# Kernel tuning notes

Hardware: AMD Instinct MI355X
Metric: run time of the kernel (lower is better)

The kernel has to match this reference:

```python
import jax, jax.numpy as jnp
import numpy as np
from jax import lax

B, CIN, IMG = 32, 3, 128   # batch, image channels, image size
D, K = 256, 512            # codebook dim, codebook size


def _conv(x, w, stride, pad):
    # PyTorch Conv2d (bias=False), NCHW / OIHW
    return lax.conv_general_dilated(x, w, (stride, stride), ((pad, pad), (pad, pad)),
                                    dimension_numbers=('NCHW', 'OIHW', 'NCHW'))


def _deconv(x, w, b):
    # PyTorch ConvTranspose2d(k=4, s=2, p=1): lhs_dilation=2, pad=k-1-p=2, flipped kernel,
    # weight layout (in, out, kh, kw) -> 'IOHW'
    y = lax.conv_general_dilated(x, jnp.flip(w, (2, 3)), (1, 1), ((2, 2), (2, 2)),
                                 lhs_dilation=(2, 2),
                                 dimension_numbers=('NCHW', 'IOHW', 'NCHW'))
    return y + b[None, :, None, None]


def _res(x, w1, w2):
    # Faithful to the source ResidualBlock: relu1 output is DISCARDED (conv1 applied to x)
    out = _conv(x, w1, 1, 1)      # 3x3, pad 1
    out = jax.nn.relu(out)
    out = _conv(out, w2, 1, 0)    # 1x1, pad 0
    return out + x


def setup_inputs() -> dict:
    key = jax.random.key(0)
    ks = jax.random.split(key, 20)
    s = 0.05
    inp = {
        'x': jax.random.uniform(ks[0], (B, CIN, IMG, IMG), jnp.float32),
        # codebook, init uniform(-1/K, 1/K) as in init_weights
        'embed_w': jax.random.uniform(ks[1], (K, D), jnp.float32, -1.0 / K, 1.0 / K),
        # encoder
        'e_w1': jax.random.normal(ks[2], (D, CIN, 4, 4), jnp.float32) * s,
        'e_w2': jax.random.normal(ks[3], (D, D, 4, 4), jnp.float32) * s,
        'e_r1a': jax.random.normal(ks[4], (D, D, 3, 3), jnp.float32) * s,
        'e_r1b': jax.random.normal(ks[5], (D, D, 1, 1), jnp.float32) * s,
        'e_r2a': jax.random.normal(ks[6], (D, D, 3, 3), jnp.float32) * s,
        'e_r2b': jax.random.normal(ks[7], (D, D, 1, 1), jnp.float32) * s,
        # decoder
        'd_r1a': jax.random.normal(ks[8], (D, D, 3, 3), jnp.float32) * s,
        'd_r1b': jax.random.normal(ks[9], (D, D, 1, 1), jnp.float32) * s,
        'd_r2a': jax.random.normal(ks[10], (D, D, 3, 3), jnp.float32) * s,
        'd_r2b': jax.random.normal(ks[11], (D, D, 1, 1), jnp.float32) * s,
        'dt1_w': jax.random.normal(ks[12], (D, D, 4, 4), jnp.float32) * s,  # (in,out,kh,kw)
        'dt1_b': jnp.zeros((D,), jnp.float32),
        'dt2_w': jax.random.normal(ks[13], (D, CIN, 4, 4), jnp.float32) * s,
        'dt2_b': jnp.zeros((CIN,), jnp.float32),
    }
    return inp


def reference(x, embed_w, e_w1, e_w2, e_r1a, e_r1b, e_r2a, e_r2b,
              d_r1a, d_r1b, d_r2a, d_r2b, dt1_w, dt1_b, dt2_w, dt2_b):
    # ---- encoder (BN layers exist but are never called in the source forward) ----
    h = jax.nn.relu(_conv(x, e_w1, 2, 1))          # (B,D,64,64)
    h = jax.nn.relu(_conv(h, e_w2, 2, 1))          # (B,D,32,32)
    h = _res(h, e_r1a, e_r1b)
    z_e = _res(h, e_r2a, e_r2b)                    # (B,D,H,W)

    # ---- vector quantisation ----
    ze = jnp.transpose(z_e, (0, 2, 3, 1))          # (B,H,W,D)
    # squared L2 distances via expansion (same argmin/values as the broadcast diff tensor)
    d2 = (jnp.sum(ze * ze, -1, keepdims=True)      # (B,H,W,1)
          - 2.0 * jnp.einsum('bhwd,kd->bhwk', ze, embed_w)
          + jnp.sum(embed_w * embed_w, -1))        # (B,H,W,K)
    dist = jnp.sqrt(jnp.maximum(d2, 0.0))          # torch.norm(p=2) before min
    idx = jnp.argmin(dist, axis=-1)                # (B,H,W)
    z_q = embed_w[idx]                             # (B,H,W,D) gather

    # losses: source averages over an extra duplicated K axis, identical to mean over B,H,W
    sg = lax.stop_gradient
    loss1 = jnp.mean(jnp.sum((ze - sg(z_q)) ** 2, -1))   # grads -> encoder
    loss2 = jnp.mean(jnp.sum((sg(ze) - z_q) ** 2, -1))   # grads -> codebook

    # ---- decoder (takes z_q; BN layers never called; relu after deconv1 only) ----
    dq = jnp.transpose(z_q, (0, 3, 1, 2))          # (B,D,H,W)
    dq = _res(dq, d_r1a, d_r1b)
    dq = _res(dq, d_r2a, d_r2b)
    dq = jax.nn.relu(_deconv(dq, dt1_w, dt1_b))    # (B,D,64,64)
    recon = jax.nn.sigmoid(_deconv(dq, dt2_w, dt2_b))  # (B,3,128,128)
    return recon, loss1, loss2
```

## Files before the change

kernel.cpp:

```cpp
#include <hip/hip_runtime.h>


typedef __attribute__((ext_vector_type(8))) short bf16x8;
typedef __attribute__((ext_vector_type(4))) float f32x4;
#define MFMA_B16(a, b, c) __builtin_amdgcn_mfma_f32_16x16x32_bf16(a, b, c, 0, 0, 0)

__device__ inline unsigned short f2b(float f) {
    unsigned int u = __float_as_uint(f);
    unsigned int r = u + 0x7fffu + ((u >> 16) & 1u);
    return (unsigned short)(r >> 16);
}
__device__ inline float b2f(unsigned short u) {
    return __uint_as_float(((unsigned int)u) << 16);
}

struct PermfArgs {
    const float* src[10];
    int kw[10];
    int so[10], si[10], sh[10], sw[10];
    int cum[11];
};

__global__ void permf_all_k(PermfArgs a, unsigned short* __restrict__ dst)
{
    int gid = blockIdx.x * 256 + threadIdx.x;
    if (gid >= a.cum[10]) return;
    int seg = 0;
    while (seg < 9 && gid >= a.cum[seg + 1]) ++seg;
    int l = gid - a.cum[seg];
    int q = l & 31;
    int n = (l >> 5) & 255;
    int rest = l >> 13;
    int cch = rest & 7;
    int khkw = rest >> 3;
    int kh = khkw / a.kw[seg], kw = khkw % a.kw[seg];
    int ci = cch * 32 + q;
    dst[gid] = f2b(a.src[seg][n * a.so[seg] + ci * a.si[seg] + kh * a.sh[seg] + kw * a.sw[seg]]);
}

__global__ void misc_prep_k(const float* __restrict__ dt2_w, unsigned short* __restrict__ wg,
                            const float* __restrict__ embed, unsigned short* __restrict__ embF,
                            const float* __restrict__ e_w1, unsigned short* __restrict__ wgc,
                            float* __restrict__ nrm, float* __restrict__ lacc)
{
    int blk = blockIdx.x, tid = threadIdx.x;
    if (blk < 48) {
        int idx = blk * 256 + tid;
        int q = idx & 31;
        int n = (idx >> 5) % 48;
        int cch = idx / (48 * 32);
        int ci = cch * 32 + q;
        int oc = n % 3, khkw = n / 3;
        int kh = khkw >> 2, kw = khkw & 3;
        wg[idx] = f2b(dt2_w[ci * 48 + oc * 16 + kh * 4 + kw]);
    } else if (blk < 560) {
        int idx = (blk - 48) * 256 + tid;
        int q = idx & 31;
        int n = (idx >> 5) & 511;
        int cch = idx >> 14;
        embF[idx] = f2b(embed[n * 256 + cch * 32 + q]);
    } else if (blk < 624) {
        int idx = (blk - 560) * 256 + tid;
        int q = idx & 31;
        int n = (idx >> 5) & 255;
        int kt = idx >> 13;
        int k = kt * 32 + q;
        float v = 0.f;
        if (k < 48) {
            int ci = k >> 4, kh = (k >> 2) & 3, kwv = k & 3;
            v = e_w1[n * 48 + ci * 16 + kh * 4 + kwv];
        }
        wgc[idx] = f2b(v);
    } else if (blk < 752) {
        int row = (blk - 624) * 4 + (tid >> 6);
        int lane = tid & 63;
        float s = 0.f;
        #pragma unroll
        for (int c = 0; c < 256; c += 64) {
            float v = embed[row * 256 + c + lane];
            s += v * v;
        }
        #pragma unroll
        for (int off = 1; off < 64; off <<= 1) s += __shfl_xor(s, off);
        if (lane == 0) nrm[row] = s;
    } else {
        if (tid == 0) lacc[0] = 0.f;
    }
}

__global__ void lossfin_k(const float* __restrict__ lacc, float* __restrict__ out)
{
    if (threadIdx.x == 0) {
        float m = lacc[0] * (1.0f / 32768.0f);
        out[1572864] = m;
        out[1572865] = m;
    }
}

__global__ void __launch_bounds__(256, 4)
conv1m_k(const float* __restrict__ x, const unsigned short* __restrict__ wgc,
         unsigned short* __restrict__ out)
{
    int bh = blockIdx.x;
    int b = bh >> 6, oh = bh & 63;
    int tid = threadIdx.x;
    int lane = tid & 63, wv = tid >> 6;
    int m = lane & 15, quad = lane >> 4;
    __shared__ float xrow[3][4][130];
    __shared__ __align__(16) unsigned short imc[64 * 72];
    for (int s = tid; s < 1560; s += 256) {
        int col = s % 130;
        int t = s / 130;
        int r = t & 3;
        int c = t >> 2;
        int ih = 2 * oh - 1 + r, iw = col - 1;
        float v = 0.f;
        if ((unsigned)ih < 128u && (unsigned)iw < 128u)
            v = x[(((b * 3 + c) << 7) + ih) * 128 + iw];
        xrow[c][r][col] = v;
    }
    __syncthreads();
    for (int s = tid; s < 4096; s += 256) {
        int px = s >> 6, k = s & 63;
        float v = 0.f;
        if (k < 48) {
            int ci = k >> 4, kh = (k >> 2) & 3, kw = k & 3;
            v = xrow[ci][kh][2 * px + kw];
        }
        imc[px * 72 + k] = f2b(v);
    }
    __syncthreads();
    f32x4 acc[16];
    f32x4 z = {0.f, 0.f, 0.f, 0.f};
    #pragma unroll
    for (int i = 0; i < 16; ++i) acc[i] = z;
    bf16x8 a0 = *(const bf16x8*)&imc[((wv << 4) + m) * 72 + (quad << 3)];
    bf16x8 a1 = *(const bf16x8*)&imc[((wv << 4) + m) * 72 + 32 + (quad << 3)];
    #pragma unroll
    for (int nt = 0; nt < 16; ++nt) {
        bf16x8 b0 = *(const bf16x8*)&wgc[(nt * 16 + m) * 32 + (quad << 3)];
        bf16x8 b1 = *(const bf16x8*)&wgc[(256 + nt * 16 + m) * 32 + (quad << 3)];
        acc[nt] = MFMA_B16(a0, b0, acc[nt]);
        acc[nt] = MFMA_B16(a1, b1, acc[nt]);
    }
    #pragma unroll
    for (int nt = 0; nt < 16; ++nt)
        #pragma unroll
        for (int r = 0; r < 4; ++r) {
            int px = (wv << 4) + quad * 4 + r;
            out[(((bh << 6) + px) << 8) + nt * 16 + (lane & 15)] = f2b(fmaxf(acc[nt][r], 0.f));
        }
}

__global__ void __launch_bounds__(256, 3)
mconv2_k(const unsigned short* __restrict__ in, const unsigned short* __restrict__ wf,
         unsigned short* __restrict__ out)
{
    int blk = blockIdx.x;
    int bb = blk >> 4, j = blk & 15;
    int lane = threadIdx.x & 63;
    int n0 = (threadIdx.x >> 6) << 6;
    int m = lane & 15, quad = lane >> 4;
    __shared__ __align__(16) unsigned short win[2 * 66 * 132];
    f32x4 acc[2][2][4];
    f32x4 z = {0.f, 0.f, 0.f, 0.f};
    #pragma unroll
    for (int a = 0; a < 2; ++a)
        #pragma unroll
        for (int i = 0; i < 2; ++i)
            #pragma unroll
            for (int t = 0; t < 4; ++t) acc[a][i][t] = z;

    for (int c0 = 0; c0 < 256; c0 += 128) {
        for (int kh = 0; kh < 4; ++kh) {
            __syncthreads();
            for (int s = threadIdx.x; s < 2 * 66 * 16; s += 256) {
                int c16 = s & 15;
                int t2 = s >> 4;
                int col = t2 % 66;
                int rr = t2 / 66;
                int ih = 4 * j - 1 + kh + 2 * rr, iw = col - 1;
                int4 v = make_int4(0, 0, 0, 0);
                if ((unsigned)ih < 64u && (unsigned)iw < 64u)
                    v = *(const int4*)&in[((((bb << 6) + ih) << 6) + iw) * 256 + c0 + (c16 << 3)];
                int cs = (col >> 1) + (col & 1) * 33;
                *(int4*)&win[(rr * 66 + cs) * 132 + (c16 << 3)] = v;
            }
            __syncthreads();
            #pragma unroll
            for (int kw = 0; kw < 4; ++kw) {
                int csoff = (kw >> 1) + (kw & 1) * 33;
                #pragma unroll
                for (int cch = 0; cch < 4; ++cch) {
                    bf16x8 a00 = *(const bf16x8*)&win[(m + csoff) * 132 + (cch << 5) + (quad << 3)];
                    bf16x8 a01 = *(const bf16x8*)&win[(m + 16 + csoff) * 132 + (cch << 5) + (quad << 3)];
                    bf16x8 a10 = *(const bf16x8*)&win[(66 + m + csoff) * 132 + (cch << 5) + (quad << 3)];
                    bf16x8 a11 = *(const bf16x8*)&win[(66 + m + 16 + csoff) * 132 + (cch << 5) + (quad << 3)];
                    int cg = (c0 >> 5) + cch;
                    int wbase = ((((kh << 2) + kw) * 8 + cg) * 256 + n0 + m) * 32 + (quad << 3);
                    bf16x8 b0 = *(const bf16x8*)&wf[wbase];
                    bf16x8 b1 = *(const bf16x8*)&wf[wbase + 16 * 32];
                    bf16x8 b2 = *(const bf16x8*)&wf[wbase + 32 * 32];
                    bf16x8 b3 = *(const bf16x8*)&wf[wbase + 48 * 32];
                    acc[0][0][0] = MFMA_B16(a00, b0, acc[0][0][0]);
                    acc[0][0][1] = MFMA_B16(a00, b1, acc[0][0][1]);
                    acc[0][0][2] = MFMA_B16(a00, b2, acc[0][0][2]);
                    acc[0][0][3] = MFMA_B16(a00, b3, acc[0][0][3]);
                    acc[0][1][0] = MFMA_B16(a01, b0, acc[0][1][0]);
                    acc[0][1][1] = MFMA_B16(a01, b1, acc[0][1][1]);
                    acc[0][1][2] = MFMA_B16(a01, b2, acc[0][1][2]);
                    acc[0][1][3] = MFMA_B16(a01, b3, acc[0][1][3]);
                    acc[1][0][0] = MFMA_B16(a10, b0, acc[1][0][0]);
                    acc[1][0][1] = MFMA_B16(a10, b1, acc[1][0][1]);
                    acc[1][0][2] = MFMA_B16(a10, b2, acc[1][0][2]);
                    acc[1][0][3] = MFMA_B16(a10, b3, acc[1][0][3]);
                    acc[1][1][0] = MFMA_B16(a11, b0, acc[1][1][0]);
                    acc[1][1][1] = MFMA_B16(a11, b1, acc[1][1][1]);
                    acc[1][1][2] = MFMA_B16(a11, b2, acc[1][1][2]);
                    acc[1][1][3] = MFMA_B16(a11, b3, acc[1][1][3]);
                }
            }
        }
    }
    #pragma unroll
    for (int row = 0; row < 2; ++row) {
        int oh = 2 * j + row;
        #pragma unroll
        for (int mt = 0; mt < 2; ++mt)
            #pragma unroll
            for (int nt = 0; nt < 4; ++nt)
                #pragma unroll
                for (int r = 0; r < 4; ++r) {
                    int px = mt * 16 + quad * 4 + r;
                    int col = n0 + nt * 16 + m;
                    out[((((bb << 5) + oh) << 5) + px) * 256 + col] = f2b(fmaxf(acc[row][mt][nt][r], 0.f));
                }
    }
}

__global__ void __launch_bounds__(256, 3)
mconv3_k(const unsigned short* __restrict__ in, const unsigned short* __restrict__ wf,
         unsigned short* __restrict__ out)
{
    int blk = blockIdx.x;
    int bb = blk >> 4, j = blk & 15;
    int lane = threadIdx.x & 63;
    int n0 = (threadIdx.x >> 6) << 6;
    int m = lane & 15, quad = lane >> 4;
    __shared__ __align__(16) unsigned short win[4 * 34 * 132];
    f32x4 acc[2][2][4];
    f32x4 z = {0.f, 0.f, 0.f, 0.f};
    #pragma unroll
    for (int a = 0; a < 2; ++a)
        #pragma unroll
        for (int i = 0; i < 2; ++i)
            #pragma unroll
            for (int t = 0; t < 4; ++t) acc[a][i][t] = z;

    for (int c0 = 0; c0 < 256; c0 += 128) {
        __syncthreads();
        for (int s = threadIdx.x; s < 4 * 34 * 16; s += 256) {
            int c16 = s & 15;
            int t2 = s >> 4;
            int col = t2 % 34;
            int rr = t2 / 34;
            int ih = 2 * j - 1 + rr, iw = col - 1;
            int4 v = make_int4(0, 0, 0, 0);
            if ((unsigned)ih < 32u && (unsigned)iw < 32u)
                v = *(const int4*)&in[((((bb << 5) + ih) << 5) + iw) * 256 + c0 + (c16 << 3)];
            *(int4*)&win[(rr * 34 + col) * 132 + (c16 << 3)] = v;
        }
        __syncthreads();
        for (int kh = 0; kh < 3; ++kh) {
            #pragma unroll
            for (int kw = 0; kw < 3; ++kw) {
                #pragma unroll
                for (int cch = 0; cch < 4; ++cch) {
                    const unsigned short* ba = &win[(kh * 34 + m + kw) * 132 + (cch << 5) + (quad << 3)];
                    bf16x8 a00 = *(const bf16x8*)ba;
                    bf16x8 a01 = *(const bf16x8*)(ba + 16 * 132);
                    bf16x8 a10 = *(const bf16x8*)(ba + 34 * 132);
                    bf16x8 a11 = *(const bf16x8*)(ba + 50 * 132);
                    int cg = (c0 >> 5) + cch;
                    int wbase = (((kh * 3 + kw) * 8 + cg) * 256 + n0 + m) * 32 + (quad << 3);
                    bf16x8 b0 = *(const bf16x8*)&wf[wbase];
                    bf16x8 b1 = *(const bf16x8*)&wf[wbase + 16 * 32];
                    bf16x8 b2 = *(const bf16x8*)&wf[wbase + 32 * 32];
                    bf16x8 b3 = *(const bf16x8*)&wf[wbase + 48 * 32];
                    acc[0][0][0] = MFMA_B16(a00, b0, acc[0][0][0]);
                    acc[0][0][1] = MFMA_B16(a00, b1, acc[0][0][1]);
                    acc[0][0][2] = MFMA_B16(a00, b2, acc[0][0][2]);
                    acc[0][0][3] = MFMA_B16(a00, b3, acc[0][0][3]);
                    acc[0][1][0] = MFMA_B16(a01, b0, acc[0][1][0]);
                    acc[0][1][1] = MFMA_B16(a01, b1, acc[0][1][1]);
                    acc[0][1][2] = MFMA_B16(a01, b2, acc[0][1][2]);
                    acc[0][1][3] = MFMA_B16(a01, b3, acc[0][1][3]);
                    acc[1][0][0] = MFMA_B16(a10, b0, acc[1][0][0]);
                    acc[1][0][1] = MFMA_B16(a10, b1, acc[1][0][1]);
                    acc[1][0][2] = MFMA_B16(a10, b2, acc[1][0][2]);
                    acc[1][0][3] = MFMA_B16(a10, b3, acc[1][0][3]);
                    acc[1][1][0] = MFMA_B16(a11, b0, acc[1][1][0]);
                    acc[1][1][1] = MFMA_B16(a11, b1, acc[1][1][1]);
                    acc[1][1][2] = MFMA_B16(a11, b2, acc[1][1][2]);
                    acc[1][1][3] = MFMA_B16(a11, b3, acc[1][1][3]);
                }
            }
        }
    }
    #pragma unroll
    for (int row = 0; row < 2; ++row) {
        int oh = 2 * j + row;
        #pragma unroll
        for (int mt = 0; mt < 2; ++mt)
            #pragma unroll
            for (int nt = 0; nt < 4; ++nt)
                #pragma unroll
                for (int r = 0; r < 4; ++r) {
                    int px = mt * 16 + quad * 4 + r;
                    int col = n0 + nt * 16 + m;
                    out[((((bb << 5) + oh) << 5) + px) * 256 + col] = f2b(fmaxf(acc[row][mt][nt][r], 0.f));
                }
    }
}

__global__ void __launch_bounds__(256, 3)
m1x1_k(const unsigned short* __restrict__ in, const unsigned short* __restrict__ wf,
       const unsigned short* __restrict__ res, unsigned short* __restrict__ outb,
       float* __restrict__ outf, int f32out)
{
    int blk = blockIdx.x;
    int lane = threadIdx.x & 63;
    int n0 = (threadIdx.x >> 6) << 6;
    int m = lane & 15, quad = lane >> 4;
    __shared__ __align__(16) unsigned short win[64 * 264];
    f32x4 acc[4][4];
    f32x4 z = {0.f, 0.f, 0.f, 0.f};
    #pragma unroll
    for (int i = 0; i < 4; ++i)
        #pragma unroll
        for (int t = 0; t < 4; ++t) acc[i][t] = z;

    int rowbase = blk << 14;
    for (int s = threadIdx.x; s < 64 * 32; s += 256) {
        int c8 = s & 31, col = s >> 5;
        *(int4*)&win[col * 264 + (c8 << 3)] = *(const int4*)&in[rowbase + (col << 8) + (c8 << 3)];
    }
    __syncthreads();
    #pragma unroll
    for (int cch = 0; cch < 8; ++cch) {
        bf16x8 a0 = *(const bf16x8*)&win[m * 264 + (cch << 5) + (quad << 3)];
        bf16x8 a1 = *(const bf16x8*)&win[(m + 16) * 264 + (cch << 5) + (quad << 3)];
        bf16x8 a2 = *(const bf16x8*)&win[(m + 32) * 264 + (cch << 5) + (quad << 3)];
        bf16x8 a3 = *(const bf16x8*)&win[(m + 48) * 264 + (cch << 5) + (quad << 3)];
        int wbase = (cch * 256 + n0 + m) * 32 + (quad << 3);
        bf16x8 b0 = *(const bf16x8*)&wf[wbase];
        bf16x8 b1 = *(const bf16x8*)&wf[wbase + 16 * 32];
        bf16x8 b2 = *(const bf16x8*)&wf[wbase + 32 * 32];
        bf16x8 b3 = *(const bf16x8*)&wf[wbase + 48 * 32];
        acc[0][0] = MFMA_B16(a0, b0, acc[0][0]);
        acc[0][1] = MFMA_B16(a0, b1, acc[0][1]);
        acc[0][2] = MFMA_B16(a0, b2, acc[0][2]);
        acc[0][3] = MFMA_B16(a0, b3, acc[0][3]);
        acc[1][0] = MFMA_B16(a1, b0, acc[1][0]);
        acc[1][1] = MFMA_B16(a1, b1, acc[1][1]);
        acc[1][2] = MFMA_B16(a1, b2, acc[1][2]);
        acc[1][3] = MFMA_B16(a1, b3, acc[1][3]);
        acc[2][0] = MFMA_B16(a2, b0, acc[2][0]);
        acc[2][1] = MFMA_B16(a2, b1, acc[2][1]);
        acc[2][2] = MFMA_B16(a2, b2, acc[2][2]);
        acc[2][3] = MFMA_B16(a2, b3, acc[2][3]);
        acc[3][0] = MFMA_B16(a3, b0, acc[3][0]);
        acc[3][1] = MFMA_B16(a3, b1, acc[3][1]);
        acc[3][2] = MFMA_B16(a3, b2, acc[3][2]);
        acc[3][3] = MFMA_B16(a3, b3, acc[3][3]);
    }
    #pragma unroll
    for (int mt = 0; mt < 4; ++mt)
        #pragma unroll
        for (int nt = 0; nt < 4; ++nt)
            #pragma unroll
            for (int r = 0; r < 4; ++r) {
                int px = mt * 16 + quad * 4 + r;
                int col = n0 + nt * 16 + m;
                int idx = rowbase + (px << 8) + col;
                float v = acc[mt][nt][r] + b2f(res[idx]);
                outb[idx] = f2b(v);
                if (f32out) outf[idx] = v;
            }
}

__global__ void __launch_bounds__(256, 3)
mdeconv1_k(const unsigned short* __restrict__ in, const unsigned short* __restrict__ wf,
           const float* __restrict__ bias, unsigned short* __restrict__ out)
{
    int blk = blockIdx.x;
    int bb = blk >> 5;
    int rem = blk & 31;
    int pp = rem >> 4;
    int i = rem & 15;
    int oy_a = pp + 4 * i;
    int p = (oy_a + 1) & 1;
    int r0a = (oy_a + 1 - p) >> 1;
    int rbase = r0a - 1;
    int lane = threadIdx.x & 63;
    int n0 = (threadIdx.x >> 6) << 6;
    int m = lane & 15, quad = lane >> 4;
    __shared__ __align__(16) unsigned short win[3 * 34 * 264];

    for (int s = threadIdx.x; s < 3 * 34 * 32; s += 256) {
        int c8 = s & 31;
        int t2 = s >> 5;
        int col = t2 % 34;
        int rr = t2 / 34;
        int ih = rbase + rr, iw = col - 1;
        int4 v = make_int4(0, 0, 0, 0);
        if ((unsigned)ih < 32u && (unsigned)iw < 32u)
            v = *(const int4*)&in[((((bb << 5) + ih) << 5) + iw) * 256 + (c8 << 3)];
        *(int4*)&win[(rr * 34 + col) * 264 + (c8 << 3)] = v;
    }
    __syncthreads();

    for (int par = 0; par < 2; ++par) {
        f32x4 acc[2][2][4];
        f32x4 z = {0.f, 0.f, 0.f, 0.f};
        #pragma unroll
        for (int a = 0; a < 2; ++a)
            #pragma unroll
            for (int i2 = 0; i2 < 2; ++i2)
                #pragma unroll
                for (int t = 0; t < 4; ++t) acc[a][i2][t] = z;

        #pragma unroll
        for (int t = 0; t < 2; ++t) {
            int kh = p + 2 * t;
            #pragma unroll
            for (int u = 0; u < 2; ++u) {
                int kw = (1 - par) + 2 * u;
                int ixoff = par - u + 1;
                #pragma unroll
                for (int cch = 0; cch < 8; ++cch) {
                    const unsigned short* baA = &win[((1 - t) * 34 + m + ixoff) * 264 + (cch << 5) + (quad << 3)];
                    const unsigned short* baB = baA + 34 * 264;
                    bf16x8 a00 = *(const bf16x8*)baA;
                    bf16x8 a01 = *(const bf16x8*)(baA + 16 * 264);
                    bf16x8 a10 = *(const bf16x8*)baB;
                    bf16x8 a11 = *(const bf16x8*)(baB + 16 * 264);
                    int wbase = ((((kh << 2) + kw) * 8 + cch) * 256 + n0 + m) * 32 + (quad << 3);
                    bf16x8 b0 = *(const bf16x8*)&wf[wbase];
                    bf16x8 b1 = *(const bf16x8*)&wf[wbase + 16 * 32];
                    bf16x8 b2 = *(const bf16x8*)&wf[wbase + 32 * 32];
                    bf16x8 b3 = *(const bf16x8*)&wf[wbase + 48 * 32];
                    acc[0][0][0] = MFMA_B16(a00, b0, acc[0][0][0]);
                    acc[0][0][1] = MFMA_B16(a00, b1, acc[0][0][1]);
                    acc[0][0][2] = MFMA_B16(a00, b2, acc[0][0][2]);
                    acc[0][0][3] = MFMA_B16(a00, b3, acc[0][0][3]);
                    acc[0][1][0] = MFMA_B16(a01, b0, acc[0][1][0]);
                    acc[0][1][1] = MFMA_B16(a01, b1, acc[0][1][1]);
                    acc[0][1][2] = MFMA_B16(a01, b2, acc[0][1][2]);
                    acc[0][1][3] = MFMA_B16(a01, b3, acc[0][1][3]);
                    acc[1][0][0] = MFMA_B16(a10, b0, acc[1][0][0]);
                    acc[1][0][1] = MFMA_B16(a10, b1, acc[1][0][1]);
                    acc[1][0][2] = MFMA_B16(a10, b2, acc[1][0][2]);
                    acc[1][0][3] = MFMA_B16(a10, b3, acc[1][0][3]);
                    acc[1][1][0] = MFMA_B16(a11, b0, acc[1][1][0]);
                    acc[1][1][1] = MFMA_B16(a11, b1, acc[1][1][1]);
                    acc[1][1][2] = MFMA_B16(a11, b2, acc[1][1][2]);
                    acc[1][1][3] = MFMA_B16(a11, b3, acc[1][1][3]);
                }
            }
        }
        #pragma unroll
        for (int row = 0; row < 2; ++row) {
            int oy = oy_a + 2 * row;
            #pragma unroll
            for (int mt = 0; mt < 2; ++mt)
                #pragma unroll
                for (int nt = 0; nt < 4; ++nt) {
                    int col = n0 + nt * 16 + m;
                    float bs = bias[col];
                    #pragma unroll
                    for (int r = 0; r < 4; ++r) {
                        int ox = 2 * (mt * 16 + quad * 4 + r) + par;
                        float v = fmaxf(acc[row][mt][nt][r] + bs, 0.f);
                        out[((((bb << 6) + oy) << 6) + ox) * 256 + col] = f2b(v);
                    }
                }
        }
    }
}

__global__ void __launch_bounds__(256, 2)
vqm_k(const unsigned short* __restrict__ zeb, const float* __restrict__ zef,
      const unsigned short* __restrict__ embF, const float* __restrict__ embed,
      const float* __restrict__ nrm, unsigned short* __restrict__ zq,
      float* __restrict__ lacc)
{
    int bh = blockIdx.x;
    int tid = threadIdx.x;
    int lane = tid & 63;
    int wv = tid >> 6;
    int m = lane & 15, quad = lane >> 4;
    __shared__ __align__(16) unsigned short win[32 * 264];
    __shared__ float bvv[4][32];
    __shared__ int   bii[4][32];
    __shared__ int   bidx[32];
    int rowbase = bh << 13;
    for (int s = tid; s < 32 * 32; s += 256) {
        int c8 = s & 31, px = s >> 5;
        *(int4*)&win[px * 264 + (c8 << 3)] = *(const int4*)&zeb[rowbase + (px << 8) + (c8 << 3)];
    }
    __syncthreads();

    f32x4 acc[2][8];
    f32x4 z = {0.f, 0.f, 0.f, 0.f};
    #pragma unroll
    for (int i = 0; i < 2; ++i)
        #pragma unroll
        for (int j = 0; j < 8; ++j) acc[i][j] = z;

    #pragma unroll
    for (int cch = 0; cch < 8; ++cch) {
        bf16x8 a0 = *(const bf16x8*)&win[m * 264 + (cch << 5) + (quad << 3)];
        bf16x8 a1 = *(const bf16x8*)&win[(m + 16) * 264 + (cch << 5) + (quad << 3)];
        #pragma unroll
        for (int nt = 0; nt < 8; ++nt) {
            bf16x8 b = *(const bf16x8*)&embF[((cch << 9) + (wv << 7) + (nt << 4) + m) * 32 + (quad << 3)];
            acc[0][nt] = MFMA_B16(a0, b, acc[0][nt]);
            acc[1][nt] = MFMA_B16(a1, b, acc[1][nt]);
        }
    }

    float nv[8];
    #pragma unroll
    for (int nt = 0; nt < 8; ++nt) nv[nt] = nrm[(wv << 7) + (nt << 4) + m];

    #pragma unroll
    for (int mt = 0; mt < 2; ++mt)
        #pragma unroll
        for (int r = 0; r < 4; ++r) {
            float bv = 1e30f;
            int bi = 0x7fffffff;
            #pragma unroll
            for (int nt = 0; nt < 8; ++nt) {
                float d = nv[nt] - 2.f * acc[mt][nt][r];
                int n = (wv << 7) + (nt << 4) + m;
                if (d < bv || (d == bv && n < bi)) { bv = d; bi = n; }
            }
            #pragma unroll
            for (int off = 1; off < 16; off <<= 1) {
                float ov = __shfl_xor(bv, off);
                int oi = __shfl_xor(bi, off);
                if (ov < bv || (ov == bv && oi < bi)) { bv = ov; bi = oi; }
            }
            if (m == 0) {
                int px = mt * 16 + quad * 4 + r;
                bvv[wv][px] = bv;
                bii[wv][px] = bi;
            }
        }
    __syncthreads();
    if (tid < 32) {
        float bv = bvv[0][tid];
        int bi = bii[0][tid];
        #pragma unroll
        for (int w2 = 1; w2 < 4; ++w2) {
            float ov = bvv[w2][tid];
            int oi = bii[w2][tid];
            if (ov < bv || (ov == bv && oi < bi)) { bv = ov; bi = oi; }
        }
        bidx[tid] = bi;
    }
    __syncthreads();

    float lsum = 0.f;
    #pragma unroll
    for (int j = 0; j < 8; ++j) {
        int px = (wv << 3) + j;
        int bi = bidx[px];
        int pix = (bh << 5) + px;
        const float4 e = *(const float4*)&embed[bi * 256 + (lane << 2)];
        const float4 zv = *(const float4*)&zef[(pix << 8) + (lane << 2)];
        ushort4 eq;
        eq.x = f2b(e.x); eq.y = f2b(e.y); eq.z = f2b(e.z); eq.w = f2b(e.w);
        *(ushort4*)&zq[(pix << 8) + (lane << 2)] = eq;
        float dx = zv.x - e.x, dy = zv.y - e.y, dz = zv.z - e.z, dw = zv.w - e.w;
        lsum += dx * dx + dy * dy + dz * dz + dw * dw;
    }
    #pragma unroll
    for (int off = 1; off < 64; off <<= 1) lsum += __shfl_xor(lsum, off);
    if (lane == 0) atomicAdd(lacc, lsum);
}

__global__ void __launch_bounds__(256, 4)
mdec2a_k(const unsigned short* __restrict__ in, const unsigned short* __restrict__ wg,
         float* __restrict__ Y)
{
    int tid = threadIdx.x;
    int lane = tid & 63;
    int wv = tid >> 6;
    int m = lane & 15, quad = lane >> 4;
    __shared__ __align__(16) unsigned short win[64 * 264];
    int pxbase = blockIdx.x << 6;
    for (int s = tid; s < 64 * 32; s += 256) {
        int c8 = s & 31, px = s >> 5;
        *(int4*)&win[px * 264 + (c8 << 3)] = *(const int4*)&in[((pxbase + px) << 8) + (c8 << 3)];
    }
    __syncthreads();
    f32x4 acc[3];
    f32x4 z = {0.f, 0.f, 0.f, 0.f};
    acc[0] = z; acc[1] = z; acc[2] = z;
    #pragma unroll
    for (int cch = 0; cch < 8; ++cch) {
        bf16x8 a = *(const bf16x8*)&win[((wv << 4) + m) * 264 + (cch << 5) + (quad << 3)];
        #pragma unroll
        for (int nt = 0; nt < 3; ++nt) {
            bf16x8 b = *(const bf16x8*)&wg[(cch * 48 + nt * 16 + m) * 32 + (quad << 3)];
            acc[nt] = MFMA_B16(a, b, acc[nt]);
        }
    }
    #pragma unroll
    for (int nt = 0; nt < 3; ++nt)
        #pragma unroll
        for (int r = 0; r < 4; ++r) {
            int px = pxbase + (wv << 4) + quad * 4 + r;
            Y[px * 48 + nt * 16 + m] = acc[nt][r];
        }
}

__global__ void dec2b_k(const float* __restrict__ Y, const float* __restrict__ bias,
                        float* __restrict__ out)
{
    int idx = blockIdx.x * 256 + threadIdx.x;
    int b = idx >> 14;
    int rem = idx & 16383;
    int oy = rem >> 7;
    int ox = rem & 127;
    int p = (oy + 1) & 1;
    int q = (ox + 1) & 1;
    float acc0 = bias[0], acc1 = bias[1], acc2 = bias[2];
    #pragma unroll
    for (int t = 0; t < 2; ++t) {
        int kh = p + 2 * t;
        int ih = (oy + 1 - kh) >> 1;
        if ((unsigned)ih >= 64u) continue;
        #pragma unroll
        for (int u = 0; u < 2; ++u) {
            int kw = q + 2 * u;
            int iw = (ox + 1 - kw) >> 1;
            if ((unsigned)iw >= 64u) continue;
            int base = ((((b << 6) + ih) << 6) + iw) * 48 + ((kh << 2) + kw) * 3;
            acc0 += Y[base];
            acc1 += Y[base + 1];
            acc2 += Y[base + 2];
        }
    }
    int obase = (b * 3 << 14) + (oy << 7) + ox;
    out[obase]           = 1.f / (1.f + expf(-acc0));
    out[obase + 16384]   = 1.f / (1.f + expf(-acc1));
    out[obase + 32768]   = 1.f / (1.f + expf(-acc2));
}

extern "C" void kernel_launch(void* const* d_in, const int* in_sizes, int n_in,
                              void* d_out, int out_size, void* d_ws, size_t ws_size,
                              hipStream_t stream)
{
    (void)in_sizes; (void)n_in; (void)out_size; (void)ws_size;
    const float* x      = (const float*)d_in[0];
    const float* embed  = (const float*)d_in[1];
    const float* e_w1   = (const float*)d_in[2];
    const float* e_w2   = (const float*)d_in[3];
    const float* e_r1a  = (const float*)d_in[4];
    const float* e_r1b  = (const float*)d_in[5];
    const float* e_r2a  = (const float*)d_in[6];
    const float* e_r2b  = (const float*)d_in[7];
    const float* d_r1a  = (const float*)d_in[8];
    const float* d_r1b  = (const float*)d_in[9];
    const float* d_r2a  = (const float*)d_in[10];
    const float* d_r2b  = (const float*)d_in[11];
    const float* dt1_w  = (const float*)d_in[12];
    const float* dt1_b  = (const float*)d_in[13];
    const float* dt2_w  = (const float*)d_in[14];
    const float* dt2_b  = (const float*)d_in[15];
    float* outp = (float*)d_out;

    char* base = (char*)d_ws;
    size_t off = 0;
    auto alloc = [&](size_t bytes) { char* p = base + off; off += (bytes + 255) & ~size_t(255); return p; };
    unsigned short* A0b = (unsigned short*)alloc(67108864);
    float*          A1f = (float*)alloc(33554432);
    unsigned short* L0  = (unsigned short*)alloc(16777216);
    unsigned short* L1  = (unsigned short*)alloc(16777216);
    unsigned short* L2  = (unsigned short*)alloc(16777216);
    unsigned short* Wf  = (unsigned short*)alloc(9437184);
    unsigned short* Wg  = (unsigned short*)alloc(24576);
    unsigned short* EmbF = (unsigned short*)alloc(262144);
    unsigned short* WgC = (unsigned short*)alloc(32768);
    float* Nrm  = (float*)alloc(2048);
    float* Lacc = (float*)alloc(64);
    float* Y = A1f;

    unsigned short* Wf_ew2  = Wf;
    unsigned short* Wf_er1a = Wf + 1048576;
    unsigned short* Wf_er1b = Wf + 1638400;
    unsigned short* Wf_er2a = Wf + 1703936;
    unsigned short* Wf_er2b = Wf + 2293760;
    unsigned short* Wf_dr1a = Wf + 2359296;
    unsigned short* Wf_dr1b = Wf + 2949120;
    unsigned short* Wf_dr2a = Wf + 3014656;
    unsigned short* Wf_dr2b = Wf + 3604480;
    unsigned short* Wf_dt1  = Wf + 3670016;

    PermfArgs pa;
    const float* srcs[10] = {e_w2, e_r1a, e_r1b, e_r2a, e_r2b, d_r1a, d_r1b, d_r2a, d_r2b, dt1_w};
    int kws[10] = {4, 3, 1, 3, 1, 3, 1, 3, 1, 4};
    int sos[10] = {4096, 2304, 256, 2304, 256, 2304, 256, 2304, 256, 16};
    int sis[10] = {16, 9, 1, 9, 1, 9, 1, 9, 1, 4096};
    int shs[10] = {4, 3, 0, 3, 0, 3, 0, 3, 0, 4};
    int sws[10] = {1, 1, 0, 1, 0, 1, 0, 1, 0, 1};
    int cums[11] = {0, 1048576, 1638400, 1703936, 2293760, 2359296,
                    2949120, 3014656, 3604480, 3670016, 4718592};
    for (int k = 0; k < 10; ++k) {
        pa.src[k] = srcs[k]; pa.kw[k] = kws[k]; pa.so[k] = sos[k];
        pa.si[k] = sis[k]; pa.sh[k] = shs[k]; pa.sw[k] = sws[k];
        pa.cum[k] = cums[k];
    }
    pa.cum[10] = cums[10];

    permf_all_k<<<18432, 256, 0, stream>>>(pa, Wf);
    misc_prep_k<<<753, 256, 0, stream>>>(dt2_w, Wg, embed, EmbF, e_w1, WgC, Nrm, Lacc);

    conv1m_k<<<32 * 64, 256, 0, stream>>>(x, WgC, A0b);
    mconv2_k<<<32 * 16, 256, 0, stream>>>(A0b, Wf_ew2, L1);
    mconv3_k<<<32 * 16, 256, 0, stream>>>(L1, Wf_er1a, L2);
    m1x1_k<<<32 * 16, 256, 0, stream>>>(L2, Wf_er1b, L1, L0, nullptr, 0);
    mconv3_k<<<32 * 16, 256, 0, stream>>>(L0, Wf_er2a, L2);
    m1x1_k<<<32 * 16, 256, 0, stream>>>(L2, Wf_er2b, L0, L1, A1f, 1);

    vqm_k<<<32 * 32, 256, 0, stream>>>(L1, A1f, EmbF, embed, Nrm, L1, Lacc);

    mconv3_k<<<32 * 16, 256, 0, stream>>>(L1, Wf_dr1a, L2);
    m1x1_k<<<32 * 16, 256, 0, stream>>>(L2, Wf_dr1b, L1, L0, nullptr, 0);
    mconv3_k<<<32 * 16, 256, 0, stream>>>(L0, Wf_dr2a, L2);
    m1x1_k<<<32 * 16, 256, 0, stream>>>(L2, Wf_dr2b, L0, L1, nullptr, 0);
    mdeconv1_k<<<32 * 32, 256, 0, stream>>>(L1, Wf_dt1, dt1_b, A0b);
    mdec2a_k<<<2048, 256, 0, stream>>>(A0b, Wg, Y);
    dec2b_k<<<2048, 256, 0, stream>>>(Y, dt2_b, outp);
    lossfin_k<<<1, 64, 0, stream>>>(Lacc, outp);
}
```

Baseline: 840.7 us.

## Fuse residual 3x3+1x1 convs, merge prep kernels, stream deconv1 rows

Fuses each residual block's 3x3 conv and 1x1 conv into a single kernel, keeping the ReLU intermediate in shared memory instead of a global L2 buffer. Merges the two weight-prep kernels into one launch and folds the loss-finalize kernel into dec2b. Also reduces deconv1's shared window from three rows to two with restaging, and raises launch-bounds occupancy hints. The intent is to cut launches and global round-trips, at the cost of higher register pressure and extra barriers in the fused kernels.

```diff
diff --git a/kernel.cpp b/kernel.cpp
--- a/kernel.cpp
+++ b/kernel.cpp
@@ -21,29 +21,31 @@
     int cum[11];
 };
 
-__global__ void permf_all_k(PermfArgs a, unsigned short* __restrict__ dst)
-{
-    int gid = blockIdx.x * 256 + threadIdx.x;
-    if (gid >= a.cum[10]) return;
-    int seg = 0;
-    while (seg < 9 && gid >= a.cum[seg + 1]) ++seg;
-    int l = gid - a.cum[seg];
-    int q = l & 31;
-    int n = (l >> 5) & 255;
-    int rest = l >> 13;
-    int cch = rest & 7;
-    int khkw = rest >> 3;
-    int kh = khkw / a.kw[seg], kw = khkw % a.kw[seg];
-    int ci = cch * 32 + q;
-    dst[gid] = f2b(a.src[seg][n * a.so[seg] + ci * a.si[seg] + kh * a.sh[seg] + kw * a.sw[seg]]);
-}
-
-__global__ void misc_prep_k(const float* __restrict__ dt2_w, unsigned short* __restrict__ wg,
-                            const float* __restrict__ embed, unsigned short* __restrict__ embF,
-                            const float* __restrict__ e_w1, unsigned short* __restrict__ wgc,
-                            float* __restrict__ nrm, float* __restrict__ lacc)
-{
-    int blk = blockIdx.x, tid = threadIdx.x;
+__global__ void prep_all_k(PermfArgs a, unsigned short* __restrict__ dst,
+                           const float* __restrict__ dt2_w, unsigned short* __restrict__ wg,
+                           const float* __restrict__ embed, unsigned short* __restrict__ embF,
+                           const float* __restrict__ e_w1, unsigned short* __restrict__ wgc,
+                           float* __restrict__ nrm, float* __restrict__ lacc)
+{
+    int blkid = blockIdx.x;
+    int tid = threadIdx.x;
+    if (blkid < 18432) {
+        int gid = blkid * 256 + tid;
+        if (gid >= a.cum[10]) return;
+        int seg = 0;
+        while (seg < 9 && gid >= a.cum[seg + 1]) ++seg;
+        int l = gid - a.cum[seg];
+        int q = l & 31;
+        int n = (l >> 5) & 255;
+        int rest = l >> 13;
+        int cch = rest & 7;
+        int khkw = rest >> 3;
+        int kh = khkw / a.kw[seg], kw = khkw % a.kw[seg];
+        int ci = cch * 32 + q;
+        dst[gid] = f2b(a.src[seg][n * a.so[seg] + ci * a.si[seg] + kh * a.sh[seg] + kw * a.sw[seg]]);
+        return;
+    }
+    int blk = blkid - 18432;
     if (blk < 48) {
         int idx = blk * 256 + tid;
         int q = idx & 31;
@@ -85,15 +87,6 @@
         if (lane == 0) nrm[row] = s;
     } else {
         if (tid == 0) lacc[0] = 0.f;
-    }
-}
-
-__global__ void lossfin_k(const float* __restrict__ lacc, float* __restrict__ out)
-{
-    if (threadIdx.x == 0) {
-        float m = lacc[0] * (1.0f / 32768.0f);
-        out[1572864] = m;
-        out[1572865] = m;
     }
 }
 
@@ -238,9 +231,10 @@
     }
 }
 
-__global__ void __launch_bounds__(256, 3)
-mconv3_k(const unsigned short* __restrict__ in, const unsigned short* __restrict__ wf,
-         unsigned short* __restrict__ out)
+__global__ void __launch_bounds__(256, 4)
+mres_k(const unsigned short* __restrict__ in, const unsigned short* __restrict__ wf3,
+       const unsigned short* __restrict__ wf1, const unsigned short* __restrict__ res,
+       unsigned short* __restrict__ outb, float* __restrict__ outf, int f32out)
 {
     int blk = blockIdx.x;
     int bb = blk >> 4, j = blk & 15;
@@ -283,10 +277,10 @@
                     bf16x8 a11 = *(const bf16x8*)(ba + 50 * 132);
                     int cg = (c0 >> 5) + cch;
                     int wbase = (((kh * 3 + kw) * 8 + cg) * 256 + n0 + m) * 32 + (quad << 3);
-                    bf16x8 b0 = *(const bf16x8*)&wf[wbase];
-                    bf16x8 b1 = *(const bf16x8*)&wf[wbase + 16 * 32];
-                    bf16x8 b2 = *(const bf16x8*)&wf[wbase + 32 * 32];
-                    bf16x8 b3 = *(const bf16x8*)&wf[wbase + 48 * 32];
+                    bf16x8 b0 = *(const bf16x8*)&wf3[wbase];
+                    bf16x8 b1 = *(const bf16x8*)&wf3[wbase + 16 * 32];
+                    bf16x8 b2 = *(const bf16x8*)&wf3[wbase + 32 * 32];
+                    bf16x8 b3 = *(const bf16x8*)&wf3[wbase + 48 * 32];
                     acc[0][0][0] = MFMA_B16(a00, b0, acc[0][0][0]);
                     acc[0][0][1] = MFMA_B16(a00, b1, acc[0][0][1]);
                     acc[0][0][2] = MFMA_B16(a00, b2, acc[0][0][2]);
@@ -307,73 +301,57 @@
             }
         }
     }
-    #pragma unroll
-    for (int row = 0; row < 2; ++row) {
-        int oh = 2 * j + row;
+
+    __syncthreads();
+    unsigned short* mid = win;
+    #pragma unroll
+    for (int row = 0; row < 2; ++row)
         #pragma unroll
         for (int mt = 0; mt < 2; ++mt)
             #pragma unroll
             for (int nt = 0; nt < 4; ++nt)
                 #pragma unroll
                 for (int r = 0; r < 4; ++r) {
-                    int px = mt * 16 + quad * 4 + r;
+                    int px = row * 32 + mt * 16 + quad * 4 + r;
                     int col = n0 + nt * 16 + m;
-                    out[((((bb << 5) + oh) << 5) + px) * 256 + col] = f2b(fmaxf(acc[row][mt][nt][r], 0.f));
+                    mid[px * 264 + col] = f2b(fmaxf(acc[row][mt][nt][r], 0.f));
                 }
-    }
-}
-
-__global__ void __launch_bounds__(256, 3)
-m1x1_k(const unsigned short* __restrict__ in, const unsigned short* __restrict__ wf,
-       const unsigned short* __restrict__ res, unsigned short* __restrict__ outb,
-       float* __restrict__ outf, int f32out)
-{
-    int blk = blockIdx.x;
-    int lane = threadIdx.x & 63;
-    int n0 = (threadIdx.x >> 6) << 6;
-    int m = lane & 15, quad = lane >> 4;
-    __shared__ __align__(16) unsigned short win[64 * 264];
-    f32x4 acc[4][4];
-    f32x4 z = {0.f, 0.f, 0.f, 0.f};
+    __syncthreads();
+
+    f32x4 acc2[4][4];
     #pragma unroll
     for (int i = 0; i < 4; ++i)
         #pragma unroll
-        for (int t = 0; t < 4; ++t) acc[i][t] = z;
-
+        for (int t = 0; t < 4; ++t) acc2[i][t] = z;
+    #pragma unroll
+    for (int cch = 0; cch < 8; ++cch) {
+        bf16x8 a0 = *(const bf16x8*)&mid[m * 264 + (cch << 5) + (quad << 3)];
+        bf16x8 a1 = *(const bf16x8*)&mid[(m + 16) * 264 + (cch << 5) + (quad << 3)];
+        bf16x8 a2 = *(const bf16x8*)&mid[(m + 32) * 264 + (cch << 5) + (quad << 3)];
+        bf16x8 a3 = *(const bf16x8*)&mid[(m + 48) * 264 + (cch << 5) + (quad << 3)];
+        int wbase = (cch * 256 + n0 + m) * 32 + (quad << 3);
+        bf16x8 b0 = *(const bf16x8*)&wf1[wbase];
+        bf16x8 b1 = *(const bf16x8*)&wf1[wbase + 16 * 32];
+        bf16x8 b2 = *(const bf16x8*)&wf1[wbase + 32 * 32];
+        bf16x8 b3 = *(const bf16x8*)&wf1[wbase + 48 * 32];
+        acc2[0][0] = MFMA_B16(a0, b0, acc2[0][0]);
+        acc2[0][1] = MFMA_B16(a0, b1, acc2[0][1]);
+        acc2[0][2] = MFMA_B16(a0, b2, acc2[0][2]);
+        acc2[0][3] = MFMA_B16(a0, b3, acc2[0][3]);
+        acc2[1][0] = MFMA_B16(a1, b0, acc2[1][0]);
+        acc2[1][1] = MFMA_B16(a1, b1, acc2[1][1]);
+        acc2[1][2] = MFMA_B16(a1, b2, acc2[1][2]);
+        acc2[1][3] = MFMA_B16(a1, b3, acc2[1][3]);
+        acc2[2][0] = MFMA_B16(a2, b0, acc2[2][0]);
+        acc2[2][1] = MFMA_B16(a2, b1, acc2[2][1]);
+        acc2[2][2] = MFMA_B16(a2, b2, acc2[2][2]);
+        acc2[2][3] = MFMA_B16(a2, b3, acc2[2][3]);
+        acc2[3][0] = MFMA_B16(a3, b0, acc2[3][0]);
+        acc2[3][1] = MFMA_B16(a3, b1, acc2[3][1]);
+        acc2[3][2] = MFMA_B16(a3, b2, acc2[3][2]);
+        acc2[3][3] = MFMA_B16(a3, b3, acc2[3][3]);
+    }
     int rowbase = blk << 14;
-    for (int s = threadIdx.x; s < 64 * 32; s += 256) {
-        int c8 = s & 31, col = s >> 5;
-        *(int4*)&win[col * 264 + (c8 << 3)] = *(const int4*)&in[rowbase + (col << 8) + (c8 << 3)];
-    }
-    __syncthreads();
-    #pragma unroll
-    for (int cch = 0; cch < 8; ++cch) {
-        bf16x8 a0 = *(const bf16x8*)&win[m * 264 + (cch << 5) + (quad << 3)];
-        bf16x8 a1 = *(const bf16x8*)&win[(m + 16) * 264 + (cch << 5) + (quad << 3)];
-        bf16x8 a2 = *(const bf16x8*)&win[(m + 32) * 264 + (cch << 5) + (quad << 3)];
-        bf16x8 a3 = *(const bf16x8*)&win[(m + 48) * 264 + (cch << 5) + (quad << 3)];
-        int wbase = (cch * 256 + n0 + m) * 32 + (quad << 3);
-        bf16x8 b0 = *(const bf16x8*)&wf[wbase];
-        bf16x8 b1 = *(const bf16x8*)&wf[wbase + 16 * 32];
-        bf16x8 b2 = *(const bf16x8*)&wf[wbase + 32 * 32];
-        bf16x8 b3 = *(const bf16x8*)&wf[wbase + 48 * 32];
-        acc[0][0] = MFMA_B16(a0, b0, acc[0][0]);
-        acc[0][1] = MFMA_B16(a0, b1, acc[0][1]);
-        acc[0][2] = MFMA_B16(a0, b2, acc[0][2]);
-        acc[0][3] = MFMA_B16(a0, b3, acc[0][3]);
-        acc[1][0] = MFMA_B16(a1, b0, acc[1][0]);
-        acc[1][1] = MFMA_B16(a1, b1, acc[1][1]);
-        acc[1][2] = MFMA_B16(a1, b2, acc[1][2]);
-        acc[1][3] = MFMA_B16(a1, b3, acc[1][3]);
-        acc[2][0] = MFMA_B16(a2, b0, acc[2][0]);
-        acc[2][1] = MFMA_B16(a2, b1, acc[2][1]);
-        acc[2][2] = MFMA_B16(a2, b2, acc[2][2]);
-        acc[2][3] = MFMA_B16(a2, b3, acc[2][3]);
-        acc[3][0] = MFMA_B16(a3, b0, acc[3][0]);
-        acc[3][1] = MFMA_B16(a3, b1, acc[3][1]);
-        acc[3][2] = MFMA_B16(a3, b2, acc[3][2]);
-        acc[3][3] = MFMA_B16(a3, b3, acc[3][3]);
-    }
     #pragma unroll
     for (int mt = 0; mt < 4; ++mt)
         #pragma unroll
@@ -383,13 +361,13 @@
                 int px = mt * 16 + quad * 4 + r;
                 int col = n0 + nt * 16 + m;
                 int idx = rowbase + (px << 8) + col;
-                float v = acc[mt][nt][r] + b2f(res[idx]);
+                float v = acc2[mt][nt][r] + b2f(res[idx]);
                 outb[idx] = f2b(v);
                 if (f32out) outf[idx] = v;
             }
 }
 
-__global__ void __launch_bounds__(256, 3)
+__global__ void __launch_bounds__(256, 4)
 mdeconv1_k(const unsigned short* __restrict__ in, const unsigned short* __restrict__ wf,
            const float* __restrict__ bias, unsigned short* __restrict__ out)
 {
@@ -405,20 +383,20 @@
     int lane = threadIdx.x & 63;
     int n0 = (threadIdx.x >> 6) << 6;
     int m = lane & 15, quad = lane >> 4;
-    __shared__ __align__(16) unsigned short win[3 * 34 * 264];
-
-    for (int s = threadIdx.x; s < 3 * 34 * 32; s += 256) {
-        int c8 = s & 31;
-        int t2 = s >> 5;
-        int col = t2 % 34;
-        int rr = t2 / 34;
-        int ih = rbase + rr, iw = col - 1;
-        int4 v = make_int4(0, 0, 0, 0);
-        if ((unsigned)ih < 32u && (unsigned)iw < 32u)
-            v = *(const int4*)&in[((((bb << 5) + ih) << 5) + iw) * 256 + (c8 << 3)];
-        *(int4*)&win[(rr * 34 + col) * 264 + (c8 << 3)] = v;
-    }
-    __syncthreads();
+    __shared__ __align__(16) unsigned short win[2 * 34 * 264];
+
+    auto stage_row = [&](int slot, int r) {
+        int ih = rbase + r;
+        for (int s = threadIdx.x; s < 34 * 32; s += 256) {
+            int c8 = s & 31;
+            int col = s >> 5;
+            int iw = col - 1;
+            int4 v = make_int4(0, 0, 0, 0);
+            if ((unsigned)ih < 32u && (unsigned)iw < 32u)
+                v = *(const int4*)&in[((((bb << 5) + ih) << 5) + iw) * 256 + (c8 << 3)];
+            *(int4*)&win[(slot * 34 + col) * 264 + (c8 << 3)] = v;
+        }
+    };
 
     for (int par = 0; par < 2; ++par) {
         f32x4 acc[2][2][4];
@@ -430,17 +408,29 @@
                 #pragma unroll
                 for (int t = 0; t < 4; ++t) acc[a][i2][t] = z;
 
-        #pragma unroll
-        for (int t = 0; t < 2; ++t) {
+        __syncthreads();
+        stage_row(0, 0);
+        if (par == 0) stage_row(1, 1);
+        __syncthreads();
+        #pragma unroll
+        for (int ph = 0; ph < 2; ++ph) {
+            int t = 1 - ph;
             int kh = p + 2 * t;
+            int slotA = ph;
+            int slotB = 1 - ph;
+            if (ph == 1) {
+                __syncthreads();
+                stage_row(0, 2);
+                __syncthreads();
+            }
             #pragma unroll
             for (int u = 0; u < 2; ++u) {
                 int kw = (1 - par) + 2 * u;
                 int ixoff = par - u + 1;
                 #pragma unroll
                 for (int cch = 0; cch < 8; ++cch) {
-                    const unsigned short* baA = &win[((1 - t) * 34 + m + ixoff) * 264 + (cch << 5) + (quad << 3)];
-                    const unsigned short* baB = baA + 34 * 264;
+                    const unsigned short* baA = &win[(slotA * 34 + m + ixoff) * 264 + (cch << 5) + (quad << 3)];
+                    const unsigned short* baB = &win[(slotB * 34 + m + ixoff) * 264 + (cch << 5) + (quad << 3)];
                     bf16x8 a00 = *(const bf16x8*)baA;
                     bf16x8 a01 = *(const bf16x8*)(baA + 16 * 264);
                     bf16x8 a10 = *(const bf16x8*)baB;
@@ -628,8 +618,13 @@
 }
 
 __global__ void dec2b_k(const float* __restrict__ Y, const float* __restrict__ bias,
-                        float* __restrict__ out)
-{
+                        const float* __restrict__ lacc, float* __restrict__ out)
+{
+    if (blockIdx.x == 0 && threadIdx.x == 0) {
+        float mloss = lacc[0] * (1.0f / 32768.0f);
+        out[1572864] = mloss;
+        out[1572865] = mloss;
+    }
     int idx = blockIdx.x * 256 + threadIdx.x;
     int b = idx >> 14;
     int rem = idx & 16383;
@@ -690,7 +685,6 @@
     float*          A1f = (float*)alloc(33554432);
     unsigned short* L0  = (unsigned short*)alloc(16777216);
     unsigned short* L1  = (unsigned short*)alloc(16777216);
-    unsigned short* L2  = (unsigned short*)alloc(16777216);
     unsigned short* Wf  = (unsigned short*)alloc(9437184);
     unsigned short* Wg  = (unsigned short*)alloc(24576);
     unsigned short* EmbF = (unsigned short*)alloc(262144);
@@ -726,24 +720,18 @@
     }
     pa.cum[10] = cums[10];
 
-    permf_all_k<<<18432, 256, 0, stream>>>(pa, Wf);
-    misc_prep_k<<<753, 256, 0, stream>>>(dt2_w, Wg, embed, EmbF, e_w1, WgC, Nrm, Lacc);
+    prep_all_k<<<19185, 256, 0, stream>>>(pa, Wf, dt2_w, Wg, embed, EmbF, e_w1, WgC, Nrm, Lacc);
 
     conv1m_k<<<32 * 64, 256, 0, stream>>>(x, WgC, A0b);
     mconv2_k<<<32 * 16, 256, 0, stream>>>(A0b, Wf_ew2, L1);
-    mconv3_k<<<32 * 16, 256, 0, stream>>>(L1, Wf_er1a, L2);
-    m1x1_k<<<32 * 16, 256, 0, stream>>>(L2, Wf_er1b, L1, L0, nullptr, 0);
-    mconv3_k<<<32 * 16, 256, 0, stream>>>(L0, Wf_er2a, L2);
-    m1x1_k<<<32 * 16, 256, 0, stream>>>(L2, Wf_er2b, L0, L1, A1f, 1);
+    mres_k<<<32 * 16, 256, 0, stream>>>(L1, Wf_er1a, Wf_er1b, L1, L0, nullptr, 0);
+    mres_k<<<32 * 16, 256, 0, stream>>>(L0, Wf_er2a, Wf_er2b, L0, L1, A1f, 1);
 
     vqm_k<<<32 * 32, 256, 0, stream>>>(L1, A1f, EmbF, embed, Nrm, L1, Lacc);
 
-    mconv3_k<<<32 * 16, 256, 0, stream>>>(L1, Wf_dr1a, L2);
-    m1x1_k<<<32 * 16, 256, 0, stream>>>(L2, Wf_dr1b, L1, L0, nullptr, 0);
-    mconv3_k<<<32 * 16, 256, 0, stream>>>(L0, Wf_dr2a, L2);
-    m1x1_k<<<32 * 16, 256, 0, stream>>>(L2, Wf_dr2b, L0, L1, nullptr, 0);
+    mres_k<<<32 * 16, 256, 0, stream>>>(L1, Wf_dr1a, Wf_dr1b, L1, L0, nullptr, 0);
+    mres_k<<<32 * 16, 256, 0, stream>>>(L0, Wf_dr2a, Wf_dr2b, L0, L1, nullptr, 0);
     mdeconv1_k<<<32 * 32, 256, 0, stream>>>(L1, Wf_dt1, dt1_b, A0b);
     mdec2a_k<<<2048, 256, 0, stream>>>(A0b, Wg, Y);
-    dec2b_k<<<2048, 256, 0, stream>>>(Y, dt2_b, outp);
-    lossfin_k<<<1, 64, 0, stream>>>(Lacc, outp);
-}
+    dec2b_k<<<2048, 256, 0, stream>>>(Y, dt2_b, Lacc, outp);
+}
```

After: 865.2 us. +2.9%, slower.
